# Optimization experiments

Measured on AMD Instinct MI355X. Metric: run time of the kernel, lower is better.

The kernel has to match this reference:

```python
import jax, jax.numpy as jnp
import numpy as np

B, S, D = 2, 512, 256      # batch, seq_len, d_model
N = 16                     # d_state
DC = 4                     # d_conv
DI = 2 * D                 # d_inner
CHUNK = 32                 # scan remat chunk size (S % CHUNK == 0)


def setup_inputs() -> dict:
    key = jax.random.key(0)
    ks = jax.random.split(key, 10)
    sc = 0.02
    return {
        "x": jax.random.normal(ks[0], (B, S, D), jnp.float32),
        "adjacency_matrix": jax.random.uniform(ks[1], (B, S, S), dtype=jnp.float32),
        "ln_w": jnp.ones((D,), jnp.float32),
        "ln_b": jnp.zeros((D,), jnp.float32),
        "W_in": jax.random.normal(ks[2], (2 * DI, D), jnp.float32) * sc,
        "conv_w": jax.random.normal(ks[3], (DI, DI, DC), jnp.float32) * sc,
        "conv_b": jnp.zeros((DI,), jnp.float32),
        "W_xp": jax.random.normal(ks[4], (2 * N + 1, DI), jnp.float32) * sc,
        "W_dt": jax.random.normal(ks[5], (DI, 1), jnp.float32) * sc,
        "b_dt": jnp.zeros((DI,), jnp.float32),
        "Wr": jax.random.normal(ks[6], (N, N), jnp.float32) * sc,
        "br": jnp.zeros((N,), jnp.float32),
        "W_out": jax.random.normal(ks[7], (D, DI), jnp.float32) * sc,
    }


def _forward(x, adj, ln_w, ln_b, W_in, conv_w, conv_b, W_xp, W_dt, b_dt, Wr, br, W_out):
    residual = x
    # LayerNorm (biased variance, eps=1e-5, matching nn.LayerNorm)
    mu = x.mean(-1, keepdims=True)
    var = ((x - mu) ** 2).mean(-1, keepdims=True)
    xn = (x - mu) * jax.lax.rsqrt(var + 1e-5) * ln_w + ln_b
    # in_proj (no bias), chunk into x branch and gate z
    xz = xn @ W_in.T                                  # [B,S,2*DI]
    xp, z = xz[..., :DI], xz[..., DI:]
    # causal-ish conv1d with padding d_conv-1, then slice to seq_len
    xc = jax.lax.conv_general_dilated(
        xp.transpose(0, 2, 1), conv_w, (1,), [(DC - 1, DC - 1)],
        dimension_numbers=("NCH", "OIH", "NCH"))
    xc = (xc + conv_b[None, :, None])[..., :S].transpose(0, 2, 1)  # [B,S,DI]
    x_act = jax.nn.silu(xc)
    # x_proj (no bias) -> delta(1), B(N), C(N)
    ssm = x_act @ W_xp.T                              # [B,S,2N+1]
    delta = jax.nn.softplus(ssm[..., :1] @ W_dt.T + b_dt)  # [B,S,DI]
    Bm, Cm = ssm[..., 1:1 + N], ssm[..., 1 + N:]      # [B,S,N]
    pos = jnp.arange(S)

    def step(carry, xs):
        h, hist = xs_carry = carry
        t, d_t, B_t, C_t, x_t, a_t = xs
        # exponential-decay state update: h [B,DI,N]
        h = h * jnp.exp(-d_t)[..., None] + x_t[..., None] * B_t[:, None, :]
        # adjacency-gated, degree-normalized aggregation over prior states
        w = a_t * (pos < t)                           # [B,S], zeros for s>=t
        deg = jnp.maximum(w.sum(-1), 1.0)             # clamp(min=1.0)
        g = jnp.einsum('bs,sbdn->bdn', w, hist) / deg[:, None, None]
        boost = 0.1 * jax.nn.silu(g @ Wr.T + br)
        # torch skips the boost when t==0 or all causal weights are zero
        h = h + jnp.where((t > 0) & jnp.any(w > 0), boost, jnp.zeros_like(boost))
        hist = hist.at[t].set(h)
        y = jnp.einsum('bdn,bn->bd', h, C_t)
        return (h, hist), y

    xs = (pos,
          delta.transpose(1, 0, 2), Bm.transpose(1, 0, 2), Cm.transpose(1, 0, 2),
          x_act.transpose(1, 0, 2), adj.transpose(1, 0, 2))
    nchunks = S // CHUNK
    xs = jax.tree_util.tree_map(lambda a: a.reshape(nchunks, CHUNK, *a.shape[1:]), xs)
    carry0 = (jnp.zeros((B, DI, N), jnp.float32),
              jnp.zeros((S, B, DI, N), jnp.float32))

    @jax.checkpoint
    def chunk_body(carry, xs_c):
        return jax.lax.scan(step, carry, xs_c)

    _, ys = jax.lax.scan(chunk_body, carry0, xs)
    y = ys.reshape(S, B, DI).transpose(1, 0, 2)       # [B,S,DI]
    return (y * jax.nn.silu(z)) @ W_out.T + residual


def reference(x, adjacency_matrix, ln_w, ln_b, W_in, conv_w, conv_b, W_xp, W_dt, b_dt, Wr, br, W_out):
    return _forward(x, adjacency_matrix, ln_w, ln_b, W_in, conv_w, conv_b,
                    W_xp, W_dt, b_dt, Wr, br, W_out)
```

## Files before the change

kernel.cpp:

```cpp
#include <hip/hip_runtime.h>
#include <math.h>

static constexpr int B  = 2;
static constexpr int S  = 512;
static constexpr int D  = 256;
static constexpr int N  = 16;
static constexpr int DI = 512;
static constexpr int CHUNK = 32;
static constexpr int NCHUNK = S / CHUNK;
static constexpr int NL2 = 4;
static constexpr int DN = DI * N;
static constexpr int NSLOT = 8;

typedef unsigned int uint32;
typedef unsigned short ushort16;
using bf16x8 = __attribute__((ext_vector_type(8))) short;
using f32x4  = __attribute__((ext_vector_type(4))) float;

__device__ __forceinline__ ushort16 f2bf(float f) {
    uint32 u = __float_as_uint(f);
    u = (u + 0x7fffu + ((u >> 16) & 1u)) >> 16;
    return (ushort16)u;
}
__device__ __forceinline__ float bflo(uint32 u) { return __uint_as_float(u << 16); }
__device__ __forceinline__ float bfhi(uint32 u) { return __uint_as_float(u & 0xffff0000u); }
__device__ __forceinline__ float bf2f(ushort16 u) { return __uint_as_float(((uint32)u) << 16); }
__device__ __forceinline__ uint32 pk2(float a, float b) {
    return (uint32)(ushort16)f2bf(a) | ((uint32)(ushort16)f2bf(b) << 16);
}
template<int K>
__device__ __forceinline__ float rork(float x) {
    return __uint_as_float((uint32)__builtin_amdgcn_mov_dpp(
        (int)__float_as_uint(x), 0x120 + K, 0xf, 0xf, false));
}
__device__ __forceinline__ size_t htIdx(int b, int dn, int sb) {
    return ((size_t)(b * (S / 32) + sb) * DN + dn) * 32;
}

__global__ void lndeg_k(const float* __restrict__ x, const float* __restrict__ w,
                        const float* __restrict__ bias, ushort16* __restrict__ xnb,
                        const float* __restrict__ adj, float* __restrict__ rdeg,
                        int* __restrict__ flagI, ushort16* __restrict__ xpb) {
    int id = blockIdx.x;
    int lane = threadIdx.x;
    if (id < B * S) {
        int row = id;
        float4 v = *(const float4*)(x + row * D + lane * 4);
        float s = v.x + v.y + v.z + v.w;
        float q = v.x * v.x + v.y * v.y + v.z * v.z + v.w * v.w;
        for (int m = 1; m < 64; m <<= 1) { s += __shfl_xor(s, m); q += __shfl_xor(q, m); }
        float mu  = s * (1.0f / D);
        float var = q * (1.0f / D) - mu * mu;
        float rs  = rsqrtf(var + 1e-5f);
        float4 wv = *(const float4*)(w + lane * 4);
        float4 bv = *(const float4*)(bias + lane * 4);
        float4 o;
        o.x = (v.x - mu) * rs * wv.x + bv.x;
        o.y = (v.y - mu) * rs * wv.y + bv.y;
        o.z = (v.z - mu) * rs * wv.z + bv.z;
        o.w = (v.w - mu) * rs * wv.w + bv.w;
        uint2 pk;
        pk.x = pk2(o.x, o.y);
        pk.y = pk2(o.z, o.w);
        *(uint2*)(xnb + row * D + lane * 4) = pk;
    } else {
        int rid = id - B * S;
        int t = rid & (S - 1), b = rid >> 9;
        const float* row = adj + ((size_t)(b * S + t)) * S;
        float s = 0.0f; bool anyp = false;
        for (int i = lane; i < t; i += 64) { float v = row[i]; s += v; anyp |= (v > 0.0f); }
        for (int m = 1; m < 64; m <<= 1) s += __shfl_xor(s, m);
        bool any = __any(anyp);
        if (lane == 0) {
            rdeg[b * S + t] = 1.0f / fmaxf(s, 1.0f);
            if (t > 0 && any) atomicOr(flagI + t, 1);
        }
        if (t < 3) {
            uint4 z = {0u, 0u, 0u, 0u};
            *(uint4*)(xpb + ((size_t)(b * (S + 3) + t)) * DI + lane * 8) = z;
        }
    }
}

template<int MODE>
__global__ __launch_bounds__(256) void gemmb_k(const ushort16* __restrict__ A,
                                               const float* __restrict__ W,
                                               const float* __restrict__ res,
                                               float* __restrict__ C,
                                               ushort16* __restrict__ xpb,
                                               float* __restrict__ zs,
                                               int M, int Nc, int K) {
    __shared__ __align__(16) short As[64 * 40];
    __shared__ __align__(16) short Ws[64 * 40];
    int tid = threadIdx.x;
    int l = tid & 63, wid = tid >> 6;
    int wm = wid & 1, wn = wid >> 1;
    int row0 = blockIdx.y * 64, col0 = blockIdx.x * 64;
    int r = tid >> 2, kseg = (tid & 3) * 8;
    f32x4 acc[2][2] = {};
    for (int k0 = 0; k0 < K; k0 += 32) {
        *(uint4*)&As[r * 40 + kseg] = *(const uint4*)(A + (size_t)(row0 + r) * K + k0 + kseg);
        {
            const float* wrow = W + (size_t)(col0 + r) * K + k0 + kseg;
            float4 w0 = *(const float4*)wrow;
            float4 w1 = *(const float4*)(wrow + 4);
            uint4 q;
            q.x = pk2(w0.x, w0.y); q.y = pk2(w0.z, w0.w);
            q.z = pk2(w1.x, w1.y); q.w = pk2(w1.z, w1.w);
            *(uint4*)&Ws[r * 40 + kseg] = q;
        }
        __syncthreads();
        bf16x8 aF[2], bF[2];
        #pragma unroll
        for (int am = 0; am < 2; ++am)
            aF[am] = *(const bf16x8*)&As[(wm * 32 + am * 16 + (l & 15)) * 40 + (l >> 4) * 8];
        #pragma unroll
        for (int bn = 0; bn < 2; ++bn)
            bF[bn] = *(const bf16x8*)&Ws[(wn * 32 + bn * 16 + (l & 15)) * 40 + (l >> 4) * 8];
        #pragma unroll
        for (int am = 0; am < 2; ++am)
            #pragma unroll
            for (int bn = 0; bn < 2; ++bn)
                acc[am][bn] = __builtin_amdgcn_mfma_f32_16x16x32_bf16(aF[am], bF[bn], acc[am][bn], 0, 0, 0);
        __syncthreads();
    }
    #pragma unroll
    for (int am = 0; am < 2; ++am)
        #pragma unroll
        for (int bn = 0; bn < 2; ++bn) {
            int cc = col0 + wn * 32 + bn * 16 + (l & 15);
            #pragma unroll
            for (int reg = 0; reg < 4; ++reg) {
                int rr = row0 + wm * 32 + am * 16 + (l >> 4) * 4 + reg;
                float v = acc[am][bn][reg];
                if (MODE == 0) {
                    if (res) v += res[(size_t)rr * Nc + cc];
                    C[(size_t)rr * Nc + cc] = v;
                } else {
                    int b = rr >> 9, t = rr & (S - 1);
                    if (cc < DI)
                        xpb[((size_t)(b * (S + 3) + 3 + t)) * DI + cc] = f2bf(v);
                    else
                        zs[((size_t)(b * S + t)) * DI + (cc - DI)] = v / (1.0f + __expf(-v));
                }
            }
        }
}

__global__ __launch_bounds__(256) void convm_k(const ushort16* __restrict__ xpb,
                                               const float* __restrict__ conv_w,
                                               const float* __restrict__ conv_b,
                                               float* __restrict__ x_act) {
    __shared__ __align__(16) short AxS[35 * 40];
    __shared__ __align__(16) short WbS[4 * 32 * 40];
    int tid = threadIdx.x;
    int l = tid & 63, wid = tid >> 6;
    int wm = wid & 1, wn = wid >> 1;
    int o0 = blockIdx.x * 32;
    int mt = blockIdx.y;
    int b = mt >> 4, tl0 = (mt & 15) * 32;
    f32x4 acc = {0.f, 0.f, 0.f, 0.f};

    for (int k0 = 0; k0 < DI; k0 += 32) {
        if (tid < 140) {
            int rr = tid >> 2, seg = tid & 3;
            uint4 v = *(const uint4*)(xpb + ((size_t)(b * (S + 3) + tl0 + rr)) * DI + k0 + seg * 8);
            *(uint4*)&AxS[rr * 40 + seg * 8] = v;
        }
        #pragma unroll
        for (int it = 0; it < 4; ++it) {
            int p = it * 256 + tid;
            int o = p >> 5, i = p & 31;
            float4 w4 = *(const float4*)(conv_w + ((size_t)(o0 + o) * DI + (k0 + i)) * 4);
            WbS[(0 * 32 + o) * 40 + i] = (short)f2bf(w4.x);
            WbS[(1 * 32 + o) * 40 + i] = (short)f2bf(w4.y);
            WbS[(2 * 32 + o) * 40 + i] = (short)f2bf(w4.z);
            WbS[(3 * 32 + o) * 40 + i] = (short)f2bf(w4.w);
        }
        __syncthreads();
        #pragma unroll
        for (int k = 0; k < 4; ++k) {
            bf16x8 aF = *(const bf16x8*)&AxS[(wm * 16 + (l & 15) + k) * 40 + (l >> 4) * 8];
            bf16x8 bF = *(const bf16x8*)&WbS[(k * 32 + wn * 16 + (l & 15)) * 40 + (l >> 4) * 8];
            acc = __builtin_amdgcn_mfma_f32_16x16x32_bf16(aF, bF, acc, 0, 0, 0);
        }
        __syncthreads();
    }
    int oc = o0 + wn * 16 + (l & 15);
    float bia = conv_b[oc];
    #pragma unroll
    for (int reg = 0; reg < 4; ++reg) {
        int m = wm * 16 + (l >> 4) * 4 + reg;
        float v = acc[reg] + bia;
        x_act[((size_t)(b * S + tl0 + m)) * DI + oc] = v / (1.0f + __expf(-v));
    }
}

__global__ void ssmE_k(const float* __restrict__ x_act, const float* __restrict__ W_xp,
                       const float* __restrict__ W_dt, const float* __restrict__ b_dt,
                       float* __restrict__ Bm, float* __restrict__ Cm,
                       float* __restrict__ E) {
    int row = blockIdx.x * 4 + (threadIdx.x >> 6);
    int lane = threadIdx.x & 63;
    const float* xr = x_act + (size_t)row * DI + lane * 8;
    float4 v0 = *(const float4*)xr;
    float4 v1 = *(const float4*)(xr + 4);
    float dtr = 0.0f;
    for (int j = 0; j < 2 * N + 1; ++j) {
        const float* wr = W_xp + (size_t)j * DI + lane * 8;
        float4 w0 = *(const float4*)wr;
        float4 w1 = *(const float4*)(wr + 4);
        float acc = v0.x * w0.x + v0.y * w0.y + v0.z * w0.z + v0.w * w0.w
                  + v1.x * w1.x + v1.y * w1.y + v1.z * w1.z + v1.w * w1.w;
        for (int m = 1; m < 64; m <<= 1) acc += __shfl_xor(acc, m);
        if (j == 0) dtr = acc;
        if (lane == 0) {
            if (j >= 1 && j < 1 + N) Bm[(size_t)row * N + (j - 1)] = acc;
            else if (j >= 1 + N)     Cm[(size_t)row * N + (j - 1 - N)] = acc;
        }
    }
    int d0 = lane * 8;
    float4 w0 = *(const float4*)(W_dt + d0);
    float4 w1 = *(const float4*)(W_dt + d0 + 4);
    float4 q0 = *(const float4*)(b_dt + d0);
    float4 q1 = *(const float4*)(b_dt + d0 + 4);
    float4 e0, e1;
    e0.x = 1.0f / (1.0f + __expf(dtr * w0.x + q0.x));
    e0.y = 1.0f / (1.0f + __expf(dtr * w0.y + q0.y));
    e0.z = 1.0f / (1.0f + __expf(dtr * w0.z + q0.z));
    e0.w = 1.0f / (1.0f + __expf(dtr * w0.w + q0.w));
    e1.x = 1.0f / (1.0f + __expf(dtr * w1.x + q1.x));
    e1.y = 1.0f / (1.0f + __expf(dtr * w1.y + q1.y));
    e1.z = 1.0f / (1.0f + __expf(dtr * w1.z + q1.z));
    e1.w = 1.0f / (1.0f + __expf(dtr * w1.w + q1.w));
    *(float4*)(E + (size_t)row * DI + d0) = e0;
    *(float4*)(E + (size_t)row * DI + d0 + 4) = e1;
}

#define SCAN32(RO, ADJT, GSUM, EL, XAL, BNL, RDEGL, FLL)                    \
    _Pragma("unroll")                                                       \
    for (int j = 0; j < CHUNK; ++j) {                                       \
        float e  = (EL) [((RO) + j) * 8 + grp];                             \
        float xa = (XAL)[((RO) + j) * 8 + grp];                             \
        float Bn = (BNL)[((RO) + j) * 16 + n];                              \
        h = h * e + xa * Bn;                                                \
        float g0 = GSUM[j], g1 = 0.f, g2 = 0.f, g3 = 0.f;                   \
        const float* ar = (ADJT) + j * 36;                                  \
        int sp = 0;                                                         \
        _Pragma("unroll")                                                   \
        for (; sp + 4 <= j; sp += 4) {                                      \
            float4 av = *(const float4*)(ar + sp);                          \
            g0 += av.x * hreg[sp];     g1 += av.y * hreg[sp + 1];           \
            g2 += av.z * hreg[sp + 2]; g3 += av.w * hreg[sp + 3];           \
        }                                                                   \
        _Pragma("unroll")                                                   \
        for (; sp < j; ++sp) g0 += ar[sp] * hreg[sp];                       \
        float gr = (g0 + g1) + (g2 + g3);                                   \
        float m0 = gr * wrr[0] + rork<4>(gr) * wrr[4]                       \
                 + rork<8>(gr) * wrr[8] + rork<12>(gr) * wrr[12];           \
        float m1 = rork<1>(gr) * wrr[1] + rork<5>(gr) * wrr[5]              \
                 + rork<9>(gr) * wrr[9] + rork<13>(gr) * wrr[13];           \
        float m2 = rork<2>(gr) * wrr[2] + rork<6>(gr) * wrr[6]              \
                 + rork<10>(gr) * wrr[10] + rork<14>(gr) * wrr[14];         \
        float m3 = rork<3>(gr) * wrr[3] + rork<7>(gr) * wrr[7]              \
                 + rork<11>(gr) * wrr[11] + rork<15>(gr) * wrr[15];         \
        float acc = fmaf((RDEGL)[(RO) + j], (m0 + m1) + (m2 + m3), brn);    \
        if ((FLL)[(RO) + j])                                                \
            h = fmaf(0.1f * acc,                                            \
                     __builtin_amdgcn_rcpf(1.0f + __expf(-acc)), h);        \
        hreg[j] = h;                                                        \
    }

#define PRESUM(GSUM, PTR) {                                                 \
    const ushort16* _p = (PTR);                                             \
    _Pragma("unroll")                                                       \
    for (int qi = 0; qi < 4; ++qi) {                                        \
        uint4 q = *(const uint4*)(_p + qi * 8);                             \
        GSUM[qi*8+0] += bflo(q.x); GSUM[qi*8+1] += bfhi(q.x);               \
        GSUM[qi*8+2] += bflo(q.y); GSUM[qi*8+3] += bfhi(q.y);               \
        GSUM[qi*8+4] += bflo(q.z); GSUM[qi*8+5] += bfhi(q.z);               \
        GSUM[qi*8+6] += bflo(q.w); GSUM[qi*8+7] += bfhi(q.w);               \
    } }

#define HWRITE(CIDX, HTBUF) {                                               \
    ushort16* ht = histT + htIdx(b, dn, (CIDX));                            \
    _Pragma("unroll")                                                       \
    for (int qi = 0; qi < 4; ++qi) {                                        \
        uint4 q;                                                            \
        q.x = pk2(hreg[qi*8+0], hreg[qi*8+1]);                              \
        q.y = pk2(hreg[qi*8+2], hreg[qi*8+3]);                              \
        q.z = pk2(hreg[qi*8+4], hreg[qi*8+5]);                              \
        q.w = pk2(hreg[qi*8+6], hreg[qi*8+7]);                              \
        *(uint4*)(ht + qi * 8) = q;                                         \
        *(uint4*)&(HTBUF)[qi * 1024 + tid * 8] = q;                         \
    } }

#define MIDPHASE(TCL) {                                                     \
    int w = tid >> 6, l = tid & 63;                                         \
    int ksg = (l >> 4) * 8;                                                 \
    f32x4 ac0[4] = {}, ac1[4] = {};                                         \
    _Pragma("unroll")                                                       \
    for (int sidx = 0; sidx < (TCL); ++sidx) {                              \
        const float* p0 = adj + ((size_t)(b * S + c0s + (TCL) * 32 + (l & 15))) * S \
                        + c0s + sidx * 32 + ksg;                            \
        const float* p1 = p0 + 16 * S;                                      \
        float4 a00 = *(const float4*)p0, a01 = *(const float4*)(p0 + 4);    \
        float4 a10 = *(const float4*)p1, a11 = *(const float4*)(p1 + 4);    \
        uint4 qa, qb;                                                       \
        qa.x = pk2(a00.x, a00.y); qa.y = pk2(a00.z, a00.w);                 \
        qa.z = pk2(a01.x, a01.y); qa.w = pk2(a01.z, a01.w);                 \
        qb.x = pk2(a10.x, a10.y); qb.y = pk2(a10.z, a10.w);                 \
        qb.z = pk2(a11.x, a11.y); qb.w = pk2(a11.z, a11.w);                 \
        bf16x8 aF0, aF1;                                                    \
        *(uint4*)&aF0 = qa; *(uint4*)&aF1 = qb;                             \
        const short* hTs = hTarr[sidx];                                     \
        _Pragma("unroll")                                                   \
        for (int dblk = 0; dblk < 4; ++dblk) {                              \
            int col = w * 64 + dblk * 16 + (l & 15);                        \
            bf16x8 bF = *(const bf16x8*)&hTs[(l >> 4) * 1024 + col * 8];    \
            ac0[dblk] = __builtin_amdgcn_mfma_f32_16x16x32_bf16(aF0, bF, ac0[dblk], 0, 0, 0); \
            ac1[dblk] = __builtin_amdgcn_mfma_f32_16x16x32_bf16(aF1, bF, ac1[dblk], 0, 0, 0); \
        }                                                                   \
    }                                                                       \
    int jb0 = (l >> 4) * 4;                                                 \
    _Pragma("unroll")                                                       \
    for (int dblk = 0; dblk < 4; ++dblk) {                                  \
        int col = w * 64 + dblk * 16 + (l & 15);                            \
        _Pragma("unroll")                                                   \
        for (int reg = 0; reg < 4; ++reg) {                                 \
            Gmid[(jb0 + reg) * 136 + col]      = (short)f2bf(ac0[dblk][reg]); \
            Gmid[(16 + jb0 + reg) * 136 + col] = (short)f2bf(ac1[dblk][reg]); \
        }                                                                   \
    } }

#define GSADD(GSUM)                                                         \
    _Pragma("unroll")                                                       \
    for (int j = 0; j < CHUNK; ++j)                                         \
        GSUM[j] += bf2f((ushort16)Gmid[j * 136 + tid]);

#define STAGEOPS(T, OFS, TRI0, TRI1, EL, XAL, BNL, RDEGL, FLL) {            \
    int j = (T) >> 3, s4 = ((T) & 7) * 4;                                   \
    {                                                                       \
        float4 a0 = *(const float4*)(adj + ((size_t)(b * S + c0s + (OFS) + j)) * S + c0s + (OFS) + s4); \
        float* dp = (TRI0) + j * 36 + s4;                                   \
        dp[0] = a0.x; dp[1] = a0.y; dp[2] = a0.z; dp[3] = a0.w;             \
    }                                                                       \
    {                                                                       \
        float4 a0 = *(const float4*)(adj + ((size_t)(b * S + c0s + (OFS) + 32 + j)) * S + c0s + (OFS) + 32 + s4); \
        float* dp = (TRI1) + j * 36 + s4;                                   \
        dp[0] = a0.x; dp[1] = a0.y; dp[2] = a0.z; dp[3] = a0.w;             \
    }                                                                       \
    int jr = (T) >> 2, dd = ((T) & 3) * 2;                                  \
    float2 ev = *(const float2*)(E     + ((size_t)(b * S + c0s + (OFS) + jr)) * DI + d0 + dd); \
    float2 xv = *(const float2*)(x_act + ((size_t)(b * S + c0s + (OFS) + jr)) * DI + d0 + dd); \
    (EL) [jr * 8 + dd] = ev.x; (EL) [jr * 8 + dd + 1] = ev.y;               \
    (XAL)[jr * 8 + dd] = xv.x; (XAL)[jr * 8 + dd + 1] = xv.y;               \
    int nn = ((T) & 3) * 4;                                                 \
    float4 bv = *(const float4*)(Bm + ((size_t)(b * S + c0s + (OFS) + jr)) * N + nn); \
    (BNL)[jr * 16 + nn] = bv.x; (BNL)[jr * 16 + nn + 1] = bv.y;             \
    (BNL)[jr * 16 + nn + 2] = bv.z; (BNL)[jr * 16 + nn + 3] = bv.w;         \
    if ((T) < 64) {                                                         \
        (RDEGL)[(T)] = rdeg[b * S + c0s + (OFS) + (T)];                     \
        (FLL)[(T)]   = flagI[c0s + (OFS) + (T)];                            \
    } }

__global__ __launch_bounds__(256) void chunk4_k(const float* __restrict__ adj,
                                                const float* __restrict__ x_act,
                                                const float* __restrict__ E,
                                                const float* __restrict__ Bm,
                                                const float* __restrict__ rdeg,
                                                const int* __restrict__ flagI,
                                                const float* __restrict__ Wr,
                                                const float* __restrict__ br,
                                                ushort16* __restrict__ Gall,
                                                ushort16* __restrict__ histT,
                                                float* __restrict__ hlast, int lc) {
    __shared__ __align__(16) char smem[69120];
    int tid = threadIdx.x;
    int c0 = 4 * lc;
    int c0s = c0 * CHUNK;
    const size_t SLOT = (size_t)B * DN * 32;
    int rp = lc & 1, wp = (lc + 1) & 1;

    if (blockIdx.x < 128) {
        float* triA   = (float*)smem;
        float* triB   = (float*)(smem + 4608);
        float* eLa    = (float*)(smem + 9216);
        float* xaLa   = (float*)(smem + 11264);
        float* BnLa   = (float*)(smem + 13312);
        float* rdegLa = (float*)(smem + 17408);
        int*   flLa   = (int*)  (smem + 17664);
        float* triC   = (float*)(smem + 17920);
        float* triD   = (float*)(smem + 22528);
        float* eLb    = (float*)(smem + 27136);
        float* xaLb   = (float*)(smem + 29184);
        float* BnLb   = (float*)(smem + 31232);
        float* rdegLb = (float*)(smem + 35328);
        int*   flLb   = (int*)  (smem + 35584);
        short* hTA    = (short*)(smem + 35840);
        short* hTB    = (short*)(smem + 44032);
        short* hTC    = (short*)(smem + 52224);
        short* Gmid   = (short*)(smem + 60416);
        short* hTD    = (short*)(smem + 60416);

        int b = blockIdx.x >> 6;
        int d0 = (blockIdx.x & 63) << 3;
        int n = tid & 15, grp = (tid >> 4) & 7;
        int d = d0 + grp;
        int dn = d * N + n;
        int dnbase = (blockIdx.x & 63) << 7;
        const short* hTarr[4] = {hTA, hTB, hTC, hTD};

        STAGEOPS(tid, 0, triA, triB, eLa, xaLa, BnLa, rdegLa, flLa)
        __syncthreads();

        float gs0[CHUNK], gs1[CHUNK];
        float wrr[16];
        float brn = 0.f, h = 0.f;
        float hreg[CHUNK];

        if (tid < 128) {
            #pragma unroll
            for (int j = 0; j < CHUNK; ++j) { gs0[j] = 0.f; gs1[j] = 0.f; }
            size_t tb = ((size_t)b * DN + dn) * 32;
            if (lc >= 2) {
                PRESUM(gs0, Gall + ((size_t)rp * NSLOT + 0) * SLOT + tb);
                PRESUM(gs1, Gall + ((size_t)rp * NSLOT + 1) * SLOT + tb);
            }
            if (lc >= 1) {
                PRESUM(gs0, Gall + ((size_t)rp * NSLOT + 4) * SLOT + tb);
                PRESUM(gs1, Gall + ((size_t)rp * NSLOT + 5) * SLOT + tb);
            }
            int probe = __builtin_amdgcn_mov_dpp((int)n, 0x121, 0xf, 0xf, false);
            bool plusdir = (probe == ((n + 1) & 15));
            #pragma unroll
            for (int k = 0; k < 16; ++k) {
                int ip = (n + k) & 15, im = (n - k + 16) & 15;
                wrr[k] = Wr[n * 16 + (plusdir ? ip : im)];
            }
            brn = br[n];
            h = (lc == 0) ? 0.0f : hlast[b * DN + dn];

            SCAN32(0, triA, gs0, eLa, xaLa, BnLa, rdegLa, flLa)
            HWRITE(c0 + 0, hTA)
        } else {
            #pragma unroll
            for (int rep = 0; rep < 2; ++rep) {
                int t2 = ((tid - 128) << 1) | rep;
                STAGEOPS(t2, 64, triC, triD, eLb, xaLb, BnLb, rdegLb, flLb)
            }
        }
        __syncthreads();
        if (tid < 128) MIDPHASE(1)
        __syncthreads();
        if (tid < 128) {
            GSADD(gs1)
            SCAN32(32, triB, gs1, eLa, xaLa, BnLa, rdegLa, flLa)
            HWRITE(c0 + 1, hTB)
        }
        __syncthreads();

        if (tid < 128) {
            #pragma unroll
            for (int j = 0; j < CHUNK; ++j) { gs0[j] = 0.f; gs1[j] = 0.f; }
            size_t tb = ((size_t)b * DN + dn) * 32;
            if (lc >= 2) {
                PRESUM(gs0, Gall + ((size_t)rp * NSLOT + 2) * SLOT + tb);
                PRESUM(gs1, Gall + ((size_t)rp * NSLOT + 3) * SLOT + tb);
            }
            if (lc >= 1) {
                PRESUM(gs0, Gall + ((size_t)rp * NSLOT + 6) * SLOT + tb);
                PRESUM(gs1, Gall + ((size_t)rp * NSLOT + 7) * SLOT + tb);
            }
            MIDPHASE(2)
        }
        __syncthreads();
        if (tid < 128) {
            GSADD(gs0)
            SCAN32(0, triC, gs0, eLb, xaLb, BnLb, rdegLb, flLb)
            HWRITE(c0 + 2, hTC)
        }
        __syncthreads();
        if (tid < 128) MIDPHASE(3)
        __syncthreads();
        if (tid < 128) GSADD(gs1)
        __syncthreads();
        if (tid < 128) {
            SCAN32(32, triD, gs1, eLb, xaLb, BnLb, rdegLb, flLb)
            HWRITE(c0 + 3, hTD)
            hlast[b * DN + dn] = h;
        }
        __syncthreads();

        if (lc < NL2 - 1) {
            int half = tid >> 7;
            int lt = tid & 127;
            int w = lt >> 6, l = lt & 63;
            int ksg = (l >> 4) * 8;
            int jb0 = (l >> 4) * 4;
            #pragma unroll
            for (int tp = 0; tp < 2; ++tp) {
                int tgt = half * 2 + tp;
                f32x4 ac0[4] = {}, ac1[4] = {};
                #pragma unroll
                for (int src = 0; src < 4; ++src) {
                    const short* hTs = hTarr[src];
                    const float* p0 = adj + ((size_t)(b * S + (4 * (lc + 1) + tgt) * 32 + (l & 15))) * S
                                    + (4 * lc + src) * 32 + ksg;
                    const float* p1 = p0 + 16 * S;
                    float4 a00 = *(const float4*)p0, a01 = *(const float4*)(p0 + 4);
                    float4 a10 = *(const float4*)p1, a11 = *(const float4*)(p1 + 4);
                    uint4 qa, qb;
                    qa.x = pk2(a00.x, a00.y); qa.y = pk2(a00.z, a00.w);
                    qa.z = pk2(a01.x, a01.y); qa.w = pk2(a01.z, a01.w);
                    qb.x = pk2(a10.x, a10.y); qb.y = pk2(a10.z, a10.w);
                    qb.z = pk2(a11.x, a11.y); qb.w = pk2(a11.z, a11.w);
                    bf16x8 aF0, aF1;
                    *(uint4*)&aF0 = qa; *(uint4*)&aF1 = qb;
                    #pragma unroll
                    for (int dblk = 0; dblk < 4; ++dblk) {
                        int col = w * 64 + dblk * 16 + (l & 15);
                        bf16x8 bF = *(const bf16x8*)&hTs[(l >> 4) * 1024 + col * 8];
                        ac0[dblk] = __builtin_amdgcn_mfma_f32_16x16x32_bf16(aF0, bF, ac0[dblk], 0, 0, 0);
                        ac1[dblk] = __builtin_amdgcn_mfma_f32_16x16x32_bf16(aF1, bF, ac1[dblk], 0, 0, 0);
                    }
                }
                ushort16* gw = Gall + ((size_t)wp * NSLOT + (4 + tgt)) * SLOT;
                #pragma unroll
                for (int dblk = 0; dblk < 4; ++dblk) {
                    int col = w * 64 + dblk * 16 + (l & 15);
                    int dng = dnbase + col;
                    uint2 o0, o1;
                    o0.x = pk2(ac0[dblk][0], ac0[dblk][1]); o0.y = pk2(ac0[dblk][2], ac0[dblk][3]);
                    o1.x = pk2(ac1[dblk][0], ac1[dblk][1]); o1.y = pk2(ac1[dblk][2], ac1[dblk][3]);
                    *(uint2*)(gw + ((size_t)b * DN + dng) * 32 + jb0) = o0;
                    *(uint2*)(gw + ((size_t)b * DN + dng) * 32 + 16 + jb0) = o1;
                }
            }
        }
    } else {
        if (lc == 0 || lc >= NL2 - 1) return;
        int idx = blockIdx.x - 128;
        int tile = idx & 63;
        int b = idx >> 6;
        int dn0 = tile * 128;
        int w = tid >> 6, l = tid & 63;
        int jh = w & 1, dh = w >> 1;
        int ksg = (l >> 4) * 8;
        int dnrow = dn0 + dh * 64 + (l & 15);
        int K = 4 * lc;
        const float* abase0 = adj + ((size_t)(b * S + (4 * (lc + 1) + 0) * CHUNK + jh * 16 + (l & 15))) * S + ksg;
        const float* abase1 = abase0 + (size_t)CHUNK * S;
        const float* abase2 = abase1 + (size_t)CHUNK * S;
        const float* abase3 = abase2 + (size_t)CHUNK * S;
        f32x4 acc[4][4] = {};
        #pragma unroll 1
        for (int ks = 0; ks < K; ++ks) {
            bf16x8 bF[4];
            #pragma unroll
            for (int dblk = 0; dblk < 4; ++dblk) {
                uint4 bP = *(const uint4*)(histT + htIdx(b, dnrow + dblk * 16, ks) + ksg);
                *(uint4*)&bF[dblk] = bP;
            }
            #pragma unroll
            for (int tgt = 0; tgt < 4; ++tgt) {
                const float* ab = (tgt == 0) ? abase0 : (tgt == 1) ? abase1
                                : (tgt == 2) ? abase2 : abase3;
                float4 af0 = *(const float4*)(ab + ks * 32);
                float4 af1 = *(const float4*)(ab + ks * 32 + 4);
                uint4 aP;
                aP.x = pk2(af0.x, af0.y); aP.y = pk2(af0.z, af0.w);
                aP.z = pk2(af1.x, af1.y); aP.w = pk2(af1.z, af1.w);
                bf16x8 aF;
                *(uint4*)&aF = aP;
                #pragma unroll
                for (int dblk = 0; dblk < 4; ++dblk)
                    acc[tgt][dblk] = __builtin_amdgcn_mfma_f32_16x16x32_bf16(aF, bF[dblk], acc[tgt][dblk], 0, 0, 0);
            }
        }
        int jb = jh * 16 + (l >> 4) * 4;
        #pragma unroll
        for (int tgt = 0; tgt < 4; ++tgt) {
            ushort16* gbase = Gall + ((size_t)wp * NSLOT + tgt) * SLOT;
            #pragma unroll
            for (int dblk = 0; dblk < 4; ++dblk) {
                int dnc = dn0 + dh * 64 + dblk * 16 + (l & 15);
                uint2 o;
                o.x = pk2(acc[tgt][dblk][0], acc[tgt][dblk][1]);
                o.y = pk2(acc[tgt][dblk][2], acc[tgt][dblk][3]);
                *(uint2*)(gbase + ((size_t)b * DN + dnc) * 32 + jb) = o;
            }
        }
    }
}

__global__ __launch_bounds__(256) void y_k(const ushort16* __restrict__ histT,
                                           const float* __restrict__ Cm,
                                           const float* __restrict__ zs,
                                           ushort16* __restrict__ yzb) {
    __shared__ float CmL[S * 17];
    int b = blockIdx.x >> 9;
    int d = blockIdx.x & (DI - 1);
    int tid = threadIdx.x;
    #pragma unroll
    for (int q = 0; q < 8; ++q) {
        int l0 = q * 1024 + tid * 4;
        int t = l0 >> 4, n0 = l0 & 15;
        float4 v = *(const float4*)(Cm + (size_t)b * S * N + l0);
        CmL[t * 17 + n0]     = v.x;
        CmL[t * 17 + n0 + 1] = v.y;
        CmL[t * 17 + n0 + 2] = v.z;
        CmL[t * 17 + n0 + 3] = v.w;
    }
    __syncthreads();
    #pragma unroll
    for (int pass = 0; pass < 2; ++pass) {
        int t = pass * 256 + tid;
        int sb = t >> 5, si = t & 31;
        const ushort16* hb = histT + htIdx(b, d * N, sb) + si;
        float a0 = 0.f, a1 = 0.f, a2 = 0.f, a3 = 0.f;
        #pragma unroll
        for (int n = 0; n < 16; n += 4) {
            a0 += bf2f(hb[(size_t)n * 32])       * CmL[t * 17 + n];
            a1 += bf2f(hb[(size_t)(n + 1) * 32]) * CmL[t * 17 + n + 1];
            a2 += bf2f(hb[(size_t)(n + 2) * 32]) * CmL[t * 17 + n + 2];
            a3 += bf2f(hb[(size_t)(n + 3) * 32]) * CmL[t * 17 + n + 3];
        }
        float acc = (a0 + a1) + (a2 + a3);
        float zv = zs[((size_t)(b * S + t)) * DI + d];
        yzb[((size_t)(b * S + t)) * DI + d] = f2bf(acc * zv);
    }
}

extern "C" void kernel_launch(void* const* d_in, const int* in_sizes, int n_in,
                              void* d_out, int out_size, void* d_ws, size_t ws_size,
                              hipStream_t stream) {
    const float* x      = (const float*)d_in[0];
    const float* adj    = (const float*)d_in[1];
    const float* ln_w   = (const float*)d_in[2];
    const float* ln_b   = (const float*)d_in[3];
    const float* W_in   = (const float*)d_in[4];
    const float* conv_w = (const float*)d_in[5];
    const float* conv_b = (const float*)d_in[6];
    const float* W_xp   = (const float*)d_in[7];
    const float* W_dt   = (const float*)d_in[8];
    const float* b_dt   = (const float*)d_in[9];
    const float* Wr     = (const float*)d_in[10];
    const float* br     = (const float*)d_in[11];
    const float* W_out  = (const float*)d_in[12];
    float* out = (float*)d_out;

    float* ws = (float*)d_ws;
    size_t off = 0;
    float* x_act  = ws + off; off += (size_t)B * S * DI;
    float* Bmb    = ws + off; off += (size_t)B * S * N;
    float* Cmb    = ws + off; off += (size_t)B * S * N;
    float* rdegp  = ws + off; off += (size_t)B * S;
    int*   flagI  = (int*)(ws + off); off += S;
    float* Ebuf   = ws + off; off += (size_t)B * S * DI;
    float* zsbuf  = ws + off; off += (size_t)B * S * DI;
    float* hlast  = ws + off; off += (size_t)B * DN;
    ushort16* xnb    = (ushort16*)(ws + off); off += (size_t)B * S * D / 2;
    ushort16* yzb    = (ushort16*)(ws + off); off += (size_t)B * S * DI / 2;
    ushort16* histT  = (ushort16*)(ws + off); off += (size_t)B * DN * S / 2;
    ushort16* Gall   = (ushort16*)(ws + off); off += (size_t)2 * NSLOT * B * DN * 32 / 2;
    ushort16* xpb    = (ushort16*)(ws + off); off += (size_t)B * (S + 3) * DI / 2;

    hipMemsetAsync(flagI, 0, S * sizeof(int), stream);

    lndeg_k<<<2 * B * S, 64, 0, stream>>>(x, ln_w, ln_b, xnb, adj, rdegp, flagI, xpb);
    gemmb_k<1><<<dim3(2 * DI / 64, B * S / 64), 256, 0, stream>>>(
        xnb, W_in, nullptr, nullptr, xpb, zsbuf, B * S, 2 * DI, D);
    convm_k<<<dim3(DI / 32, B * S / 32), 256, 0, stream>>>(xpb, conv_w, conv_b, x_act);
    ssmE_k<<<B * S / 4, 256, 0, stream>>>(x_act, W_xp, W_dt, b_dt, Bmb, Cmb, Ebuf);

    for (int lc = 0; lc < NL2; ++lc)
        chunk4_k<<<256, 256, 0, stream>>>(adj, x_act, Ebuf, Bmb, rdegp, flagI,
                                          Wr, br, Gall, histT, hlast, lc);

    y_k<<<B * DI, 256, 0, stream>>>(histT, Cmb, zsbuf, yzb);

    gemmb_k<0><<<dim3(D / 64, B * S / 64), 256, 0, stream>>>(
        yzb, W_out, x, out, nullptr, nullptr, B * S, D, DI);
}
```

Measured before the change: 250.5 us.

## Overlap mid-phase MFMA source contributions with scans using idle warps

```diff
diff --git a/kernel.cpp b/kernel.cpp
--- a/kernel.cpp
+++ b/kernel.cpp
@@ -295,13 +295,14 @@
         *(uint4*)&(HTBUF)[qi * 1024 + tid * 8] = q;                         \
     } }
 
-#define MIDPHASE(TCL) {                                                     \
-    int w = tid >> 6, l = tid & 63;                                         \
+#define MIDSRC(TGT, S0v, S1v, GM) {                                         \
+    int lt = tid & 127;                                                     \
+    int w = lt >> 6, l = lt & 63;                                           \
     int ksg = (l >> 4) * 8;                                                 \
     f32x4 ac0[4] = {}, ac1[4] = {};                                         \
     _Pragma("unroll")                                                       \
-    for (int sidx = 0; sidx < (TCL); ++sidx) {                              \
-        const float* p0 = adj + ((size_t)(b * S + c0s + (TCL) * 32 + (l & 15))) * S \
+    for (int sidx = (S0v); sidx < (S1v); ++sidx) {                          \
+        const float* p0 = adj + ((size_t)(b * S + c0s + (TGT) * 32 + (l & 15))) * S \
                         + c0s + sidx * 32 + ksg;                            \
         const float* p1 = p0 + 16 * S;                                      \
         float4 a00 = *(const float4*)p0, a01 = *(const float4*)(p0 + 4);    \
@@ -328,15 +329,21 @@
         int col = w * 64 + dblk * 16 + (l & 15);                            \
         _Pragma("unroll")                                                   \
         for (int reg = 0; reg < 4; ++reg) {                                 \
-            Gmid[(jb0 + reg) * 136 + col]      = (short)f2bf(ac0[dblk][reg]); \
-            Gmid[(16 + jb0 + reg) * 136 + col] = (short)f2bf(ac1[dblk][reg]); \
+            (GM)[(jb0 + reg) * 136 + col]      = (short)f2bf(ac0[dblk][reg]); \
+            (GM)[(16 + jb0 + reg) * 136 + col] = (short)f2bf(ac1[dblk][reg]); \
         }                                                                   \
     } }
 
-#define GSADD(GSUM)                                                         \
+#define GSADD1(GSUM, GM)                                                    \
     _Pragma("unroll")                                                       \
     for (int j = 0; j < CHUNK; ++j)                                         \
-        GSUM[j] += bf2f((ushort16)Gmid[j * 136 + tid]);
+        GSUM[j] += bf2f((ushort16)(GM)[j * 136 + tid]);
+
+#define GSADD2(GSUM, GM1, GM2)                                              \
+    _Pragma("unroll")                                                       \
+    for (int j = 0; j < CHUNK; ++j)                                         \
+        GSUM[j] += bf2f((ushort16)(GM1)[j * 136 + tid])                     \
+                 + bf2f((ushort16)(GM2)[j * 136 + tid]);
 
 #define STAGEOPS(T, OFS, TRI0, TRI1, EL, XAL, BNL, RDEGL, FLL) {            \
     int j = (T) >> 3, s4 = ((T) & 7) * 4;                                   \
@@ -375,7 +382,7 @@
                                                 ushort16* __restrict__ Gall,
                                                 ushort16* __restrict__ histT,
                                                 float* __restrict__ hlast, int lc) {
-    __shared__ __align__(16) char smem[69120];
+    __shared__ __align__(16) char smem[94720];
     int tid = threadIdx.x;
     int c0 = 4 * lc;
     int c0s = c0 * CHUNK;
@@ -400,8 +407,10 @@
         short* hTA    = (short*)(smem + 35840);
         short* hTB    = (short*)(smem + 44032);
         short* hTC    = (short*)(smem + 52224);
-        short* Gmid   = (short*)(smem + 60416);
         short* hTD    = (short*)(smem + 60416);
+        short* GmidB  = (short*)(smem + 68608);
+        short* GmidC  = (short*)(smem + 77312);
+        short* GmidD  = (short*)(smem + 86016);
 
         int b = blockIdx.x >> 6;
         int d0 = (blockIdx.x & 63) << 3;
@@ -451,12 +460,16 @@
             }
         }
         __syncthreads();
-        if (tid < 128) MIDPHASE(1)
-        __syncthreads();
+
+        if (tid < 128) MIDSRC(1, 0, 1, GmidB)
+        __syncthreads();
+
         if (tid < 128) {
-            GSADD(gs1)
+            GSADD1(gs1, GmidB)
             SCAN32(32, triB, gs1, eLa, xaLa, BnLa, rdegLa, flLa)
             HWRITE(c0 + 1, hTB)
+        } else {
+            MIDSRC(2, 0, 1, GmidC)
         }
         __syncthreads();
 
@@ -472,20 +485,24 @@
                 PRESUM(gs0, Gall + ((size_t)rp * NSLOT + 6) * SLOT + tb);
                 PRESUM(gs1, Gall + ((size_t)rp * NSLOT + 7) * SLOT + tb);
             }
-            MIDPHASE(2)
-        }
-        __syncthreads();
+            MIDSRC(2, 1, 2, GmidB)
+        } else {
+            MIDSRC(3, 0, 2, GmidD)
+        }
+        __syncthreads();
+
         if (tid < 128) {
-            GSADD(gs0)
+            GSADD2(gs0, GmidC, GmidB)
             SCAN32(0, triC, gs0, eLb, xaLb, BnLb, rdegLb, flLb)
             HWRITE(c0 + 2, hTC)
         }
         __syncthreads();
-        if (tid < 128) MIDPHASE(3)
-        __syncthreads();
-        if (tid < 128) GSADD(gs1)
-        __syncthreads();
+
+        if (tid < 128) MIDSRC(3, 2, 3, GmidB)
+        __syncthreads();
+
         if (tid < 128) {
+            GSADD2(gs1, GmidD, GmidB)
             SCAN32(32, triD, gs1, eLb, xaLb, BnLb, rdegLb, flLb)
             HWRITE(c0 + 3, hTD)
             hlast[b * DN + dn] = h;
```

After: 250.4 us. Within noise of the previous version (-0.1%).
